# Performance work log

Measured on AMD Instinct MI355X. Metric: run time of the kernel, lower is better.

Reference implementation:

```python
import jax, jax.numpy as jnp
import numpy as np


def _scan_dir(x, A, B, reverse):
    """First-order linear recurrence h_i = A*h_{i-1} + B*x_i along last axis (W).
    x: [Bsz, C, H, W]; A, B: [C]. reverse=True scans right-to-left but returns
    states in original index order (matching torch scan_backward)."""
    xs = jnp.moveaxis(x, -1, 0)  # [W, Bsz, C, H]
    Ab = A[None, :, None]
    Bb = B[None, :, None]
    def step(h, xi):
        h = Ab * h + Bb * xi
        return h, h
    h0 = jnp.zeros_like(xs[0])
    _, hs = jax.lax.scan(step, h0, xs, reverse=reverse)
    return jnp.moveaxis(hs, 0, -1)  # [Bsz, C, H, W]


def _conv1x1(x, W, b):
    # x: [B,Cin,H,W], W: [Cout,Cin], b: [Cout]
    return jnp.einsum('bchw,dc->bdhw', x, W) + b[None, :, None, None]


def setup_inputs() -> dict:
    key = jax.random.key(0)
    ks = jax.random.split(key, 10)
    B, C, H, W = 8, 64, 128, 128
    D = 128  # hidden_dim
    return {
        'F_in': jax.random.normal(ks[0], (B, C, H, W), dtype=jnp.float32),
        'prior': jax.random.uniform(ks[1], (B, 1, H, W), dtype=jnp.float32),
        'Wi': jax.random.normal(ks[2], (D, C), dtype=jnp.float32) * 0.05,
        'bi': jnp.zeros((D,), dtype=jnp.float32),
        'A_param': jax.random.normal(ks[3], (D,), dtype=jnp.float32),
        'B_param': jax.random.normal(ks[4], (D,), dtype=jnp.float32),
        'alpha': jnp.float32(0.1),
        'gamma': jnp.float32(0.1),
        'Wf': jax.random.normal(ks[5], (D, 4 * D), dtype=jnp.float32) * 0.05,
        'bf': jnp.zeros((D,), dtype=jnp.float32),
        'Wo': jax.random.normal(ks[6], (C, D), dtype=jnp.float32) * 0.05,
        'bo': jnp.zeros((C,), dtype=jnp.float32),
    }


def reference(F_in, prior, Wi, bi, A_param, B_param, alpha, gamma, Wf, bf, Wo, bo):
    # prior has 1 channel, repeated to C channels (prior already matches HxW)
    prior_r = jnp.broadcast_to(prior, F_in.shape)
    F_mod = F_in + alpha * prior_r
    x = _conv1x1(F_mod, Wi, bi)  # [B, D, H, W]
    A = jnp.tanh(A_param)
    Bp = B_param
    h_lr = _scan_dir(x, A, Bp, reverse=False)
    h_rl = _scan_dir(x, A, Bp, reverse=True)
    xt = jnp.swapaxes(x, 2, 3)  # scan over H axis
    h_tb = jnp.swapaxes(_scan_dir(xt, A, Bp, reverse=False), 2, 3)
    h_bt = jnp.swapaxes(_scan_dir(xt, A, Bp, reverse=True), 2, 3)
    h = jnp.concatenate([h_lr, h_rl, h_tb, h_bt], axis=1)  # [B, 4D, H, W]
    h = _conv1x1(h, Wf, bf)   # fusion -> [B, D, H, W]
    out = _conv1x1(h, Wo, bo)  # output_proj -> [B, C, H, W]
    return F_mod + gamma * out
```

## Files before the change

kernel.cpp:

```cpp
#include <hip/hip_runtime.h>
#include <hip/hip_bf16.h>

typedef unsigned int u32;
typedef unsigned short u16;
typedef float f32x2 __attribute__((ext_vector_type(2)));
typedef float f32x4 __attribute__((ext_vector_type(4)));
using bf16x8 = __attribute__((ext_vector_type(8))) short;
using f32x4v = __attribute__((ext_vector_type(4))) float;

#define DEVINL __device__ __forceinline__

constexpr int LDS_A = 65536;
constexpr int LDS_B = 32768;
constexpr int XS = 132;
constexpr int LDS_X = 128 * XS * 2;

DEVINL float bf2f(u16 u) { union { u32 i; float f; } v; v.i = ((u32)u) << 16; return v.f; }
DEVINL float bf2f_lo(u32 u) { union { u32 i; float f; } v; v.i = u << 16; return v.f; }
DEVINL float bf2f_hi(u32 u) { union { u32 i; float f; } v; v.i = u & 0xffff0000u; return v.f; }
DEVINL u16 f2bf(float f) {
  __hip_bfloat16 h = __float2bfloat16(f);
  u16 r; __builtin_memcpy(&r, &h, 2); return r;
}
DEVINL u32 pack2(float a, float b) { return (u32)f2bf(a) | ((u32)f2bf(b) << 16); }

__global__ __launch_bounds__(256) void k_pre(
    const float* __restrict__ Wf, const float* __restrict__ Wo,
    const float* __restrict__ bf_, const float* __restrict__ bo,
    const float* __restrict__ A_param, const float* __restrict__ Wi,
    float* __restrict__ A_t, float* __restrict__ beff,
    u16* __restrict__ Mrow, u16* __restrict__ Wi_bf) {
  const int wg = blockIdx.x, t = threadIdx.x;
  if (wg < 128) {
    const int idx = wg * 256 + t;
    const int cout = idx >> 9;
    const int k = idx & 511;
    float s = 0.f;
    for (int d = 0; d < 128; ++d) s = fmaf(Wo[cout * 128 + d], Wf[d * 512 + k], s);
    const int dir = k >> 7, dm = k & 127;
    Mrow[(dir * 64 + cout) * 128 + dm] = f2bf(s);
  } else if (wg == 128) {
    if (t < 128) A_t[t] = tanhf(A_param[t]);
    if (t < 64) {
      float s = bo[t];
      for (int d = 0; d < 128; ++d) s = fmaf(Wo[t * 128 + d], bf_[d], s);
      beff[t] = s;
    }
  } else {
#pragma unroll
    for (int k = 0; k < 32; ++k) {
      const int i = t + k * 256;
      Wi_bf[i] = f2bf(Wi[i]);
    }
  }
}

extern __shared__ char smem[];

template <bool REV, int ROWB>
DEVINL void scan_local(char* buf, int dp, int chunk, f32x2 A2) {
  f32x2 h = { 0.f, 0.f };
  const u32 cb = (u32)(dp * 4);
  const int s = chunk * 32;
  u32 nx[8];
#pragma unroll
  for (int j = 0; j < 8; ++j) {
    const int i = REV ? (127 - (s + j)) : (s + j);
    nx[j] = *(const u32*)(buf + i * ROWB + (cb ^ ((u32)((i & 7) << 4))));
  }
  for (int ib = 0; ib < 32; ib += 8) {
    u32 cur[8];
#pragma unroll
    for (int j = 0; j < 8; ++j) cur[j] = nx[j];
    if (ib + 8 < 32) {
#pragma unroll
      for (int j = 0; j < 8; ++j) {
        const int i2 = s + ib + 8 + j;
        const int i = REV ? (127 - i2) : i2;
        nx[j] = *(const u32*)(buf + i * ROWB + (cb ^ ((u32)((i & 7) << 4))));
      }
    }
#pragma unroll
    for (int j = 0; j < 8; ++j) {
      const int i2 = s + ib + j;
      const int i = REV ? (127 - i2) : i2;
      const f32x2 xv = { bf2f_lo(cur[j]), bf2f_hi(cur[j]) };
      h = A2 * h + xv;
      *(u32*)(buf + i * ROWB + (cb ^ ((u32)((i & 7) << 4)))) = pack2(h.x, h.y);
    }
  }
}

template <bool REV, int ROWB>
DEVINL void scan_fix(char* buf, int dp, int chunk, f32x2 A2) {
  if (chunk == 0) return;
  f32x2 q = A2;
#pragma unroll
  for (int k = 0; k < 5; ++k) q *= q;
  const u32 cb = (u32)(dp * 4);
  f32x2 C = { 0.f, 0.f };
  for (int k = 0; k < chunk; ++k) {
    const int i2 = k * 32 + 31;
    const int i = REV ? (127 - i2) : i2;
    const u32 v = *(const u32*)(buf + i * ROWB + (cb ^ ((u32)((i & 7) << 4))));
    const f32x2 xv = { bf2f_lo(v), bf2f_hi(v) };
    C = C * q + xv;
  }
  f32x2 p = A2;
  const int s = chunk * 32;
  u32 nx[8];
#pragma unroll
  for (int j = 0; j < 8; ++j) {
    const int i = REV ? (127 - (s + j)) : (s + j);
    nx[j] = *(const u32*)(buf + i * ROWB + (cb ^ ((u32)((i & 7) << 4))));
  }
  for (int ib = 0; ib < 32; ib += 8) {
    u32 cur[8];
#pragma unroll
    for (int j = 0; j < 8; ++j) cur[j] = nx[j];
    if (ib + 8 < 32) {
#pragma unroll
      for (int j = 0; j < 8; ++j) {
        const int i2 = s + ib + 8 + j;
        const int i = REV ? (127 - i2) : i2;
        nx[j] = *(const u32*)(buf + i * ROWB + (cb ^ ((u32)((i & 7) << 4))));
      }
    }
#pragma unroll
    for (int j = 0; j < 8; ++j) {
      const int i2 = s + ib + j;
      const int i = REV ? (127 - i2) : i2;
      const f32x2 xv = { bf2f_lo(cur[j]), bf2f_hi(cur[j]) };
      const f32x2 hv = p * C + xv;
      *(u32*)(buf + i * ROWB + (cb ^ ((u32)((i & 7) << 4)))) = pack2(hv.x, hv.y);
      p *= A2;
    }
  }
}

__global__ __launch_bounds__(512, 4) void k_A(
    const float* __restrict__ F_in, const float* __restrict__ prior,
    const u16* __restrict__ Wi_bf, const float* __restrict__ bi,
    const float* __restrict__ Bp, const float* __restrict__ alpha_p,
    const float* __restrict__ A_t, const u16* __restrict__ Mrow,
    u16* __restrict__ x2, u16* __restrict__ Shp) {
  char* bufA = smem;
  char* bufB = smem + 32768;

  const int t = threadIdx.x;
  const int lane = t & 63, wv = t >> 6;
  const int l15 = lane & 15, kg = lane >> 4;
  const int bid = blockIdx.x, b = bid >> 7, h = bid & 127;
  const int wq = wv & 3, eh = wv >> 2;

  {
    const int w = t & 127, ch = t >> 7;
    const float alpha = alpha_p[0];
    const float pv = prior[(b * 128 + h) * 128 + w];
    const float* Fb = F_in + ((size_t)b * 64 + ch * 16) * 16384 + h * 128 + w;
    const u32 sw = (u32)((w & 7) << 4);
    char* rowp = bufA + w * 256;
#pragma unroll
    for (int q = 0; q < 2; ++q) {
      float fv[8];
#pragma unroll
      for (int j = 0; j < 8; ++j) fv[j] = fmaf(alpha, pv, Fb[(q * 8 + j) * 16384]);
      uint4 pk;
      pk.x = pack2(fv[0], fv[1]); pk.y = pack2(fv[2], fv[3]);
      pk.z = pack2(fv[4], fv[5]); pk.w = pack2(fv[6], fv[7]);
      *(uint4*)(rowp + ((u32)(ch * 32 + q * 16) ^ sw)) = pk;
    }
  }
  __syncthreads();

  bf16x8 bF[2][2];
#pragma unroll
  for (int wj = 0; wj < 2; ++wj)
#pragma unroll
    for (int ks = 0; ks < 2; ++ks) {
      const int row = wq * 32 + wj * 16 + l15;
      bF[wj][ks] = *(const bf16x8*)(bufA + row * 256 + ((u32)(ks * 64 + kg * 16) ^ ((u32)((row & 7) << 4))));
    }
  __syncthreads();

  {
    f32x4v acc[4][2];
#pragma unroll
    for (int dt = 0; dt < 4; ++dt) {
      const f32x4 bv = *(const f32x4*)(bi + eh * 64 + dt * 16 + kg * 4);
      const f32x4v bvv = { bv.x, bv.y, bv.z, bv.w };
#pragma unroll
      for (int wj = 0; wj < 2; ++wj) acc[dt][wj] = bvv;
    }
#pragma unroll
    for (int ks = 0; ks < 2; ++ks)
#pragma unroll
      for (int dt = 0; dt < 4; ++dt) {
        const bf16x8 aWi = *(const bf16x8*)(Wi_bf + (eh * 64 + dt * 16 + l15) * 64 + ks * 32 + kg * 8);
        acc[dt][0] = __builtin_amdgcn_mfma_f32_16x16x32_bf16(aWi, bF[0][ks], acc[dt][0], 0, 0, 0);
        acc[dt][1] = __builtin_amdgcn_mfma_f32_16x16x32_bf16(aWi, bF[1][ks], acc[dt][1], 0, 0, 0);
      }
#pragma unroll
    for (int dt = 0; dt < 4; ++dt) {
      const f32x4 B4 = *(const f32x4*)(Bp + eh * 64 + dt * 16 + kg * 4);
      const f32x4v B4v = { B4.x, B4.y, B4.z, B4.w };
#pragma unroll
      for (int wj = 0; wj < 2; ++wj) {
        const f32x4v sv = acc[dt][wj] * B4v;
        const int w = wq * 32 + wj * 16 + l15;
        const int dl = eh * 64 + dt * 16 + kg * 4;
        uint2 pk;
        pk.x = pack2(sv[0], sv[1]);
        pk.y = pack2(sv[2], sv[3]);
        const u32 col = (u32)(dl * 2) ^ ((u32)((w & 7) << 4));
        *(uint2*)(bufA + w * 256 + col) = pk;
        *(uint2*)(bufB + w * 256 + col) = pk;
      }
    }
  }
  __syncthreads();

  {
    u16* xg = x2 + (size_t)bid * 16384;
#pragma unroll
    for (int j = 0; j < 4; ++j) {
      const int idx = t + j * 512;
      const int row = idx >> 4, q = idx & 15;
      const uint4 v = *(const uint4*)(bufA + row * 256 + ((u32)(q * 16) ^ ((u32)((row & 7) << 4))));
      *(uint4*)(xg + row * 128 + q * 8) = v;
    }
  }
  __syncthreads();

  {
    const int sub = t & 255, dp = sub & 63, chunk = sub >> 6, dir = t >> 8;
    const f32x2 a = *(const f32x2*)(A_t + dp * 2);
    char* sb = dir ? bufB : bufA;
    if (dir == 0) scan_local<false, 256>(sb, dp, chunk, a);
    else          scan_local<true , 256>(sb, dp, chunk, a);
    __syncthreads();
    if (dir == 0) scan_fix<false, 256>(sb, dp, chunk, a);
    else          scan_fix<true , 256>(sb, dp, chunk, a);
  }
  __syncthreads();

  f32x4v acc2[2][2];
#pragma unroll
  for (int i = 0; i < 2; ++i)
#pragma unroll
    for (int j = 0; j < 2; ++j) acc2[i][j] = (f32x4v)0.f;
#pragma unroll
  for (int dir = 0; dir < 2; ++dir) {
    const char* buf = dir ? bufB : bufA;
#pragma unroll
    for (int ks = 0; ks < 4; ++ks) {
      bf16x8 afr[2], bfr[2];
#pragma unroll
      for (int ct = 0; ct < 2; ++ct)
        afr[ct] = *(const bf16x8*)(Mrow + ((size_t)dir * 64 + eh * 32 + ct * 16 + l15) * 128 + ks * 32 + kg * 8);
#pragma unroll
      for (int pt = 0; pt < 2; ++pt) {
        const int row = wq * 32 + pt * 16 + l15;
        bfr[pt] = *(const bf16x8*)(buf + row * 256 + ((u32)(ks * 64 + kg * 16) ^ ((u32)((row & 7) << 4))));
      }
#pragma unroll
      for (int ct = 0; ct < 2; ++ct)
#pragma unroll
        for (int pt = 0; pt < 2; ++pt)
          acc2[ct][pt] = __builtin_amdgcn_mfma_f32_16x16x32_bf16(bfr[pt], afr[ct], acc2[ct][pt], 0, 0, 0);
    }
  }
  __syncthreads();

#pragma unroll
  for (int ct = 0; ct < 2; ++ct)
#pragma unroll
    for (int pt = 0; pt < 2; ++pt) {
      const int c = eh * 32 + ct * 16 + l15;
      const int pos = wq * 32 + pt * 16 + kg * 4;
      *(f32x4v*)(smem + c * 512 + ((u32)(pos * 4) ^ ((u32)((c & 7) << 4)))) = acc2[ct][pt];
    }
  __syncthreads();

  {
    u16* og = Shp + (size_t)bid * 8192;
#pragma unroll
    for (int j = 0; j < 8; ++j) {
      const int i = t + j * 512;
      const int c = i >> 6, p2 = (i & 63) * 2;
      const f32x2 v = *(const f32x2*)(smem + c * 512 + ((u32)(p2 * 4) ^ ((u32)((c & 7) << 4))));
      *(u32*)(og + c * 128 + p2) = pack2(v.x, v.y);
    }
  }
}

__global__ __launch_bounds__(256, 5) void k_B(
    const u16* __restrict__ x2,
    const float* __restrict__ A_t, const u16* __restrict__ Mrow,
    u16* __restrict__ Svp) {
  char* bufA = smem;
  char* bufB = smem + 16384;
  const int t = threadIdx.x;
  const int lane = t & 63, wv = t >> 6, l15 = lane & 15, kg = lane >> 4;
  const int bid = blockIdx.x;
  const int b = bid >> 8, w = (bid >> 1) & 127, e = bid & 1;

#pragma unroll
  for (int j = 0; j < 4; ++j) {
    const int idx = t + j * 256;
    const int hh = idx >> 3, q = idx & 7;
    const uint4 v = *(const uint4*)(x2 + ((size_t)(b * 128 + hh) * 128 + w) * 128 + e * 64 + q * 8);
    const u32 col = (u32)(q * 16) ^ ((u32)((hh & 7) << 4));
    *(uint4*)(bufA + hh * 128 + col) = v;
    *(uint4*)(bufB + hh * 128 + col) = v;
  }
  __syncthreads();

  {
    const int dp = t & 31, chunk = (t >> 5) & 3, dir = t >> 7;
    const f32x2 a = *(const f32x2*)(A_t + e * 64 + dp * 2);
    char* sb = dir ? bufB : bufA;
    if (dir == 0) scan_local<false, 128>(sb, dp, chunk, a);
    else          scan_local<true , 128>(sb, dp, chunk, a);
    __syncthreads();
    if (dir == 0) scan_fix<false, 128>(sb, dp, chunk, a);
    else          scan_fix<true , 128>(sb, dp, chunk, a);
  }
  __syncthreads();

  f32x4v acc2[4][2];
#pragma unroll
  for (int i = 0; i < 4; ++i)
#pragma unroll
    for (int j = 0; j < 2; ++j) acc2[i][j] = (f32x4v)0.f;
#pragma unroll
  for (int dir = 0; dir < 2; ++dir) {
    const char* buf = dir ? bufB : bufA;
#pragma unroll
    for (int ks = 0; ks < 2; ++ks) {
      bf16x8 afr[4], bfr[2];
#pragma unroll
      for (int ct = 0; ct < 4; ++ct)
        afr[ct] = *(const bf16x8*)(Mrow + ((size_t)(dir + 2) * 64 + ct * 16 + l15) * 128 + e * 64 + ks * 32 + kg * 8);
#pragma unroll
      for (int pt = 0; pt < 2; ++pt) {
        const int row = wv * 32 + pt * 16 + l15;
        bfr[pt] = *(const bf16x8*)(buf + row * 128 + ((u32)(ks * 64 + kg * 16) ^ ((u32)((row & 7) << 4))));
      }
#pragma unroll
      for (int ct = 0; ct < 4; ++ct)
#pragma unroll
        for (int pt = 0; pt < 2; ++pt)
          acc2[ct][pt] = __builtin_amdgcn_mfma_f32_16x16x32_bf16(bfr[pt], afr[ct], acc2[ct][pt], 0, 0, 0);
    }
  }
  __syncthreads();

#pragma unroll
  for (int ct = 0; ct < 4; ++ct)
#pragma unroll
    for (int pt = 0; pt < 2; ++pt) {
      const int c = ct * 16 + l15;
      const int pos = wv * 32 + pt * 16 + kg * 4;
      *(f32x4v*)(smem + c * 512 + ((u32)(pos * 4) ^ ((u32)((c & 7) << 4)))) = acc2[ct][pt];
    }
  __syncthreads();

  {
    u16* og = Svp + (size_t)bid * 8192;
#pragma unroll
    for (int j = 0; j < 16; ++j) {
      const int i = t + j * 256;
      const int c = i >> 6, p2 = (i & 63) * 2;
      const f32x2 v = *(const f32x2*)(smem + c * 512 + ((u32)(p2 * 4) ^ ((u32)((c & 7) << 4))));
      *(u32*)(og + c * 128 + p2) = pack2(v.x, v.y);
    }
  }
}

__global__ __launch_bounds__(256) void k_final(
    const float* __restrict__ F_in, const float* __restrict__ prior,
    const float* __restrict__ alpha_p, const float* __restrict__ gamma_p,
    const float* __restrict__ beff, const u16* __restrict__ Svp,
    const u16* __restrict__ Shp, float* __restrict__ out) {
  u16* Xu = (u16*)smem;
  const int t = threadIdx.x;
  const int bid = blockIdx.x, b = bid >> 6, c = bid & 63;
  const size_t base = (size_t)bid * 16384;

  for (int i = t; i < 2048; i += 256) {
    const int w = i >> 4, q = i & 15;
    const u16* s0 = Svp + ((size_t)((b * 128 + w) * 2)) * 8192 + c * 128 + q * 8;
    const uint4 a4 = *(const uint4*)(s0);
    const uint4 b4 = *(const uint4*)(s0 + 8192);
    const u16* ap = (const u16*)&a4;
    const u16* bp = (const u16*)&b4;
    u32* dst = (u32*)(Xu + w * 132 + q * 8);
#pragma unroll
    for (int k = 0; k < 4; ++k) {
      const float lo = bf2f(ap[k * 2]) + bf2f(bp[k * 2]);
      const float hi = bf2f(ap[k * 2 + 1]) + bf2f(bp[k * 2 + 1]);
      dst[k] = pack2(lo, hi);
    }
  }
  __syncthreads();
  const float alpha = alpha_p[0], gamma = gamma_p[0];
  const float be = beff[c];
  for (int i = t; i < 2048; i += 256) {
    const int hh = i >> 4, w8 = (i & 15) * 8;
    const size_t off = base + hh * 128 + w8;
    const u16* sh0 = Shp + (size_t)(b * 128 + hh) * 8192 + c * 128 + w8;
    const uint4 g0 = *(const uint4*)(sh0);
    const u16* p0 = (const u16*)&g0;
    const float* Fp = F_in + off;
    float* Op = out + off;
    const float* Pp = prior + (b * 128 + hh) * 128 + w8;
#pragma unroll
    for (int q = 0; q < 8; ++q) {
      const float sv = bf2f(Xu[(w8 + q) * 132 + hh]);
      Op[q] = Fp[q] + alpha * Pp[q] + gamma * (bf2f(p0[q]) + sv + be);
    }
  }
}

extern "C" void kernel_launch(void* const* d_in, const int* in_sizes, int n_in,
                              void* d_out, int out_size, void* d_ws, size_t ws_size,
                              hipStream_t stream) {
  const float* F_in   = (const float*)d_in[0];
  const float* prior  = (const float*)d_in[1];
  const float* Wi     = (const float*)d_in[2];
  const float* bi     = (const float*)d_in[3];
  const float* A_par  = (const float*)d_in[4];
  const float* B_par  = (const float*)d_in[5];
  const float* alpha  = (const float*)d_in[6];
  const float* gamma  = (const float*)d_in[7];
  const float* Wf     = (const float*)d_in[8];
  const float* bf_    = (const float*)d_in[9];
  const float* Wo     = (const float*)d_in[10];
  const float* bo     = (const float*)d_in[11];
  float* out = (float*)d_out;

  char* ws = (char*)d_ws;
  float* A_t   = (float*)ws;
  float* beff  = (float*)(ws + 512);
  u16*   Mrow  = (u16*)(ws + 1024);
  u16*   Wi_bf = (u16*)(ws + 66560);
  u16*   x2    = (u16*)(ws + 82944);
  u16*   Shp   = (u16*)(ws + 82944 + 33554432);
  u16*   Svp   = (u16*)(ws + 82944 + 67108864);

  hipFuncSetAttribute((const void*)k_A, hipFuncAttributeMaxDynamicSharedMemorySize, LDS_A);
  hipFuncSetAttribute((const void*)k_B, hipFuncAttributeMaxDynamicSharedMemorySize, LDS_B);

  k_pre  <<<130, 256, 0, stream>>>(Wf, Wo, bf_, bo, A_par, Wi, A_t, beff, Mrow, Wi_bf);
  k_A    <<<1024, 512, LDS_A, stream>>>(F_in, prior, Wi_bf, bi, B_par, alpha, A_t, Mrow, x2, Shp);
  k_B    <<<2048, 256, LDS_B, stream>>>(x2, A_t, Mrow, Svp);
  k_final<<<512, 256, LDS_X, stream>>>(F_in, prior, alpha, gamma, beff, Svp, Shp, out);
}
```

Measured before the change: 96.86 us.

## Process full hidden dim per block in vertical scan kernel, drop partial-sum merge

The vertical-scan kernel k_B now uses 512-thread blocks that each handle all 128 hidden channels of a column, instead of two 256-thread blocks each handling half the channels and writing separate partial projections. The channel reduction in the projection GEMM is now done entirely inside one block, so Svp holds one bf16 partial instead of two and the final kernel reads half as much Svp data with no add-and-repack. Shared helpers for the scan, GEMM and epilogue are factored out and reused by both kernels. The trade-off is fewer, larger blocks with twice the LDS each, which may lower occupancy.

```diff
diff --git a/kernel.cpp b/kernel.cpp
--- a/kernel.cpp
+++ b/kernel.cpp
@@ -10,8 +10,7 @@
 
 #define DEVINL __device__ __forceinline__
 
-constexpr int LDS_A = 65536;
-constexpr int LDS_B = 32768;
+constexpr int LDS_AB = 65536;
 constexpr int XS = 132;
 constexpr int LDS_X = 128 * XS * 2;
 
@@ -57,7 +56,7 @@
 
 extern __shared__ char smem[];
 
-template <bool REV, int ROWB>
+template <bool REV>
 DEVINL void scan_local(char* buf, int dp, int chunk, f32x2 A2) {
   f32x2 h = { 0.f, 0.f };
   const u32 cb = (u32)(dp * 4);
@@ -66,7 +65,7 @@
 #pragma unroll
   for (int j = 0; j < 8; ++j) {
     const int i = REV ? (127 - (s + j)) : (s + j);
-    nx[j] = *(const u32*)(buf + i * ROWB + (cb ^ ((u32)((i & 7) << 4))));
+    nx[j] = *(const u32*)(buf + i * 256 + (cb ^ ((u32)((i & 7) << 4))));
   }
   for (int ib = 0; ib < 32; ib += 8) {
     u32 cur[8];
@@ -77,7 +76,7 @@
       for (int j = 0; j < 8; ++j) {
         const int i2 = s + ib + 8 + j;
         const int i = REV ? (127 - i2) : i2;
-        nx[j] = *(const u32*)(buf + i * ROWB + (cb ^ ((u32)((i & 7) << 4))));
+        nx[j] = *(const u32*)(buf + i * 256 + (cb ^ ((u32)((i & 7) << 4))));
       }
     }
 #pragma unroll
@@ -86,12 +85,12 @@
       const int i = REV ? (127 - i2) : i2;
       const f32x2 xv = { bf2f_lo(cur[j]), bf2f_hi(cur[j]) };
       h = A2 * h + xv;
-      *(u32*)(buf + i * ROWB + (cb ^ ((u32)((i & 7) << 4)))) = pack2(h.x, h.y);
-    }
-  }
-}
-
-template <bool REV, int ROWB>
+      *(u32*)(buf + i * 256 + (cb ^ ((u32)((i & 7) << 4)))) = pack2(h.x, h.y);
+    }
+  }
+}
+
+template <bool REV>
 DEVINL void scan_fix(char* buf, int dp, int chunk, f32x2 A2) {
   if (chunk == 0) return;
   f32x2 q = A2;
@@ -102,7 +101,7 @@
   for (int k = 0; k < chunk; ++k) {
     const int i2 = k * 32 + 31;
     const int i = REV ? (127 - i2) : i2;
-    const u32 v = *(const u32*)(buf + i * ROWB + (cb ^ ((u32)((i & 7) << 4))));
+    const u32 v = *(const u32*)(buf + i * 256 + (cb ^ ((u32)((i & 7) << 4))));
     const f32x2 xv = { bf2f_lo(v), bf2f_hi(v) };
     C = C * q + xv;
   }
@@ -112,7 +111,7 @@
 #pragma unroll
   for (int j = 0; j < 8; ++j) {
     const int i = REV ? (127 - (s + j)) : (s + j);
-    nx[j] = *(const u32*)(buf + i * ROWB + (cb ^ ((u32)((i & 7) << 4))));
+    nx[j] = *(const u32*)(buf + i * 256 + (cb ^ ((u32)((i & 7) << 4))));
   }
   for (int ib = 0; ib < 32; ib += 8) {
     u32 cur[8];
@@ -123,7 +122,7 @@
       for (int j = 0; j < 8; ++j) {
         const int i2 = s + ib + 8 + j;
         const int i = REV ? (127 - i2) : i2;
-        nx[j] = *(const u32*)(buf + i * ROWB + (cb ^ ((u32)((i & 7) << 4))));
+        nx[j] = *(const u32*)(buf + i * 256 + (cb ^ ((u32)((i & 7) << 4))));
       }
     }
 #pragma unroll
@@ -132,9 +131,66 @@
       const int i = REV ? (127 - i2) : i2;
       const f32x2 xv = { bf2f_lo(cur[j]), bf2f_hi(cur[j]) };
       const f32x2 hv = p * C + xv;
-      *(u32*)(buf + i * ROWB + (cb ^ ((u32)((i & 7) << 4)))) = pack2(hv.x, hv.y);
+      *(u32*)(buf + i * 256 + (cb ^ ((u32)((i & 7) << 4)))) = pack2(hv.x, hv.y);
       p *= A2;
     }
+  }
+}
+
+DEVINL void run_scans512(char* bufA, char* bufB, int t, const float* __restrict__ A_t) {
+  const int sub = t & 255, dp = sub & 63, chunk = sub >> 6, dir = t >> 8;
+  const f32x2 a = *(const f32x2*)(A_t + dp * 2);
+  char* sb = dir ? bufB : bufA;
+  if (dir == 0) scan_local<false>(sb, dp, chunk, a);
+  else          scan_local<true >(sb, dp, chunk, a);
+  __syncthreads();
+  if (dir == 0) scan_fix<false>(sb, dp, chunk, a);
+  else          scan_fix<true >(sb, dp, chunk, a);
+}
+
+DEVINL void combine_full(const char* bufA, const char* bufB, const u16* __restrict__ Mrow,
+                         int dir_base, int eh, int wq, int l15, int kg,
+                         f32x4v (&acc2)[2][2]) {
+#pragma unroll
+  for (int dir = 0; dir < 2; ++dir) {
+    const char* buf = dir ? bufB : bufA;
+#pragma unroll
+    for (int ks = 0; ks < 4; ++ks) {
+      bf16x8 afr[2], bfr[2];
+#pragma unroll
+      for (int ct = 0; ct < 2; ++ct)
+        afr[ct] = *(const bf16x8*)(Mrow + ((size_t)(dir_base + dir) * 64 + eh * 32 + ct * 16 + l15) * 128 + ks * 32 + kg * 8);
+#pragma unroll
+      for (int pt = 0; pt < 2; ++pt) {
+        const int row = wq * 32 + pt * 16 + l15;
+        bfr[pt] = *(const bf16x8*)(buf + row * 256 + ((u32)(ks * 64 + kg * 16) ^ ((u32)((row & 7) << 4))));
+      }
+#pragma unroll
+      for (int ct = 0; ct < 2; ++ct)
+#pragma unroll
+        for (int pt = 0; pt < 2; ++pt)
+          acc2[ct][pt] = __builtin_amdgcn_mfma_f32_16x16x32_bf16(bfr[pt], afr[ct], acc2[ct][pt], 0, 0, 0);
+    }
+  }
+}
+
+DEVINL void outs_epilogue512(const f32x4v (&acc2)[2][2], int eh, int wq, int l15, int kg,
+                             int t, u16* __restrict__ og) {
+#pragma unroll
+  for (int ct = 0; ct < 2; ++ct)
+#pragma unroll
+    for (int pt = 0; pt < 2; ++pt) {
+      const int c = eh * 32 + ct * 16 + l15;
+      const int pos = wq * 32 + pt * 16 + kg * 4;
+      *(f32x4v*)(smem + c * 512 + ((u32)(pos * 4) ^ ((u32)((c & 7) << 4)))) = acc2[ct][pt];
+    }
+  __syncthreads();
+#pragma unroll
+  for (int j = 0; j < 8; ++j) {
+    const int i = t + j * 512;
+    const int c = i >> 6, p2 = (i & 63) * 2;
+    const f32x2 v = *(const f32x2*)(smem + c * 512 + ((u32)(p2 * 4) ^ ((u32)((c & 7) << 4))));
+    *(u32*)(og + c * 128 + p2) = pack2(v.x, v.y);
   }
 }
 
@@ -232,16 +288,7 @@
   }
   __syncthreads();
 
-  {
-    const int sub = t & 255, dp = sub & 63, chunk = sub >> 6, dir = t >> 8;
-    const f32x2 a = *(const f32x2*)(A_t + dp * 2);
-    char* sb = dir ? bufB : bufA;
-    if (dir == 0) scan_local<false, 256>(sb, dp, chunk, a);
-    else          scan_local<true , 256>(sb, dp, chunk, a);
-    __syncthreads();
-    if (dir == 0) scan_fix<false, 256>(sb, dp, chunk, a);
-    else          scan_fix<true , 256>(sb, dp, chunk, a);
-  }
+  run_scans512(bufA, bufB, t, A_t);
   __syncthreads();
 
   f32x4v acc2[2][2];
@@ -249,133 +296,46 @@
   for (int i = 0; i < 2; ++i)
 #pragma unroll
     for (int j = 0; j < 2; ++j) acc2[i][j] = (f32x4v)0.f;
-#pragma unroll
-  for (int dir = 0; dir < 2; ++dir) {
-    const char* buf = dir ? bufB : bufA;
-#pragma unroll
-    for (int ks = 0; ks < 4; ++ks) {
-      bf16x8 afr[2], bfr[2];
-#pragma unroll
-      for (int ct = 0; ct < 2; ++ct)
-        afr[ct] = *(const bf16x8*)(Mrow + ((size_t)dir * 64 + eh * 32 + ct * 16 + l15) * 128 + ks * 32 + kg * 8);
-#pragma unroll
-      for (int pt = 0; pt < 2; ++pt) {
-        const int row = wq * 32 + pt * 16 + l15;
-        bfr[pt] = *(const bf16x8*)(buf + row * 256 + ((u32)(ks * 64 + kg * 16) ^ ((u32)((row & 7) << 4))));
-      }
-#pragma unroll
-      for (int ct = 0; ct < 2; ++ct)
-#pragma unroll
-        for (int pt = 0; pt < 2; ++pt)
-          acc2[ct][pt] = __builtin_amdgcn_mfma_f32_16x16x32_bf16(bfr[pt], afr[ct], acc2[ct][pt], 0, 0, 0);
-    }
-  }
-  __syncthreads();
-
-#pragma unroll
-  for (int ct = 0; ct < 2; ++ct)
-#pragma unroll
-    for (int pt = 0; pt < 2; ++pt) {
-      const int c = eh * 32 + ct * 16 + l15;
-      const int pos = wq * 32 + pt * 16 + kg * 4;
-      *(f32x4v*)(smem + c * 512 + ((u32)(pos * 4) ^ ((u32)((c & 7) << 4)))) = acc2[ct][pt];
-    }
-  __syncthreads();
-
-  {
-    u16* og = Shp + (size_t)bid * 8192;
-#pragma unroll
-    for (int j = 0; j < 8; ++j) {
-      const int i = t + j * 512;
-      const int c = i >> 6, p2 = (i & 63) * 2;
-      const f32x2 v = *(const f32x2*)(smem + c * 512 + ((u32)(p2 * 4) ^ ((u32)((c & 7) << 4))));
-      *(u32*)(og + c * 128 + p2) = pack2(v.x, v.y);
-    }
-  }
-}
-
-__global__ __launch_bounds__(256, 5) void k_B(
+  combine_full(bufA, bufB, Mrow, 0, eh, wq, l15, kg, acc2);
+  __syncthreads();
+  outs_epilogue512(acc2, eh, wq, l15, kg, t, Shp + (size_t)bid * 8192);
+}
+
+__global__ __launch_bounds__(512, 4) void k_B(
     const u16* __restrict__ x2,
     const float* __restrict__ A_t, const u16* __restrict__ Mrow,
     u16* __restrict__ Svp) {
   char* bufA = smem;
-  char* bufB = smem + 16384;
+  char* bufB = smem + 32768;
+
   const int t = threadIdx.x;
-  const int lane = t & 63, wv = t >> 6, l15 = lane & 15, kg = lane >> 4;
-  const int bid = blockIdx.x;
-  const int b = bid >> 8, w = (bid >> 1) & 127, e = bid & 1;
+  const int lane = t & 63, wv = t >> 6;
+  const int l15 = lane & 15, kg = lane >> 4;
+  const int bid = blockIdx.x, b = bid >> 7, w = bid & 127;
+  const int wq = wv & 3, eh = wv >> 2;
 
 #pragma unroll
   for (int j = 0; j < 4; ++j) {
-    const int idx = t + j * 256;
-    const int hh = idx >> 3, q = idx & 7;
-    const uint4 v = *(const uint4*)(x2 + ((size_t)(b * 128 + hh) * 128 + w) * 128 + e * 64 + q * 8);
+    const int idx = t + j * 512;
+    const int hh = idx >> 4, q = idx & 15;
+    const uint4 v = *(const uint4*)(x2 + ((size_t)(b * 128 + hh) * 128 + w) * 128 + q * 8);
     const u32 col = (u32)(q * 16) ^ ((u32)((hh & 7) << 4));
-    *(uint4*)(bufA + hh * 128 + col) = v;
-    *(uint4*)(bufB + hh * 128 + col) = v;
-  }
-  __syncthreads();
-
-  {
-    const int dp = t & 31, chunk = (t >> 5) & 3, dir = t >> 7;
-    const f32x2 a = *(const f32x2*)(A_t + e * 64 + dp * 2);
-    char* sb = dir ? bufB : bufA;
-    if (dir == 0) scan_local<false, 128>(sb, dp, chunk, a);
-    else          scan_local<true , 128>(sb, dp, chunk, a);
-    __syncthreads();
-    if (dir == 0) scan_fix<false, 128>(sb, dp, chunk, a);
-    else          scan_fix<true , 128>(sb, dp, chunk, a);
-  }
-  __syncthreads();
-
-  f32x4v acc2[4][2];
-#pragma unroll
-  for (int i = 0; i < 4; ++i)
+    *(uint4*)(bufA + hh * 256 + col) = v;
+    *(uint4*)(bufB + hh * 256 + col) = v;
+  }
+  __syncthreads();
+
+  run_scans512(bufA, bufB, t, A_t);
+  __syncthreads();
+
+  f32x4v acc2[2][2];
+#pragma unroll
+  for (int i = 0; i < 2; ++i)
 #pragma unroll
     for (int j = 0; j < 2; ++j) acc2[i][j] = (f32x4v)0.f;
-#pragma unroll
-  for (int dir = 0; dir < 2; ++dir) {
-    const char* buf = dir ? bufB : bufA;
-#pragma unroll
-    for (int ks = 0; ks < 2; ++ks) {
-      bf16x8 afr[4], bfr[2];
-#pragma unroll
-      for (int ct = 0; ct < 4; ++ct)
-        afr[ct] = *(const bf16x8*)(Mrow + ((size_t)(dir + 2) * 64 + ct * 16 + l15) * 128 + e * 64 + ks * 32 + kg * 8);
-#pragma unroll
-      for (int pt = 0; pt < 2; ++pt) {
-        const int row = wv * 32 + pt * 16 + l15;
-        bfr[pt] = *(const bf16x8*)(buf + row * 128 + ((u32)(ks * 64 + kg * 16) ^ ((u32)((row & 7) << 4))));
-      }
-#pragma unroll
-      for (int ct = 0; ct < 4; ++ct)
-#pragma unroll
-        for (int pt = 0; pt < 2; ++pt)
-          acc2[ct][pt] = __builtin_amdgcn_mfma_f32_16x16x32_bf16(bfr[pt], afr[ct], acc2[ct][pt], 0, 0, 0);
-    }
-  }
-  __syncthreads();
-
-#pragma unroll
-  for (int ct = 0; ct < 4; ++ct)
-#pragma unroll
-    for (int pt = 0; pt < 2; ++pt) {
-      const int c = ct * 16 + l15;
-      const int pos = wv * 32 + pt * 16 + kg * 4;
-      *(f32x4v*)(smem + c * 512 + ((u32)(pos * 4) ^ ((u32)((c & 7) << 4)))) = acc2[ct][pt];
-    }
-  __syncthreads();
-
-  {
-    u16* og = Svp + (size_t)bid * 8192;
-#pragma unroll
-    for (int j = 0; j < 16; ++j) {
-      const int i = t + j * 256;
-      const int c = i >> 6, p2 = (i & 63) * 2;
-      const f32x2 v = *(const f32x2*)(smem + c * 512 + ((u32)(p2 * 4) ^ ((u32)((c & 7) << 4))));
-      *(u32*)(og + c * 128 + p2) = pack2(v.x, v.y);
-    }
-  }
+  combine_full(bufA, bufB, Mrow, 2, eh, wq, l15, kg, acc2);
+  __syncthreads();
+  outs_epilogue512(acc2, eh, wq, l15, kg, t, Svp + (size_t)bid * 8192);
 }
 
 __global__ __launch_bounds__(256) void k_final(
@@ -390,18 +350,9 @@
 
   for (int i = t; i < 2048; i += 256) {
     const int w = i >> 4, q = i & 15;
-    const u16* s0 = Svp + ((size_t)((b * 128 + w) * 2)) * 8192 + c * 128 + q * 8;
-    const uint4 a4 = *(const uint4*)(s0);
-    const uint4 b4 = *(const uint4*)(s0 + 8192);
-    const u16* ap = (const u16*)&a4;
-    const u16* bp = (const u16*)&b4;
+    const uint4 a4 = *(const uint4*)(Svp + (size_t)(b * 128 + w) * 8192 + c * 128 + q * 8);
     u32* dst = (u32*)(Xu + w * 132 + q * 8);
-#pragma unroll
-    for (int k = 0; k < 4; ++k) {
-      const float lo = bf2f(ap[k * 2]) + bf2f(bp[k * 2]);
-      const float hi = bf2f(ap[k * 2 + 1]) + bf2f(bp[k * 2 + 1]);
-      dst[k] = pack2(lo, hi);
-    }
+    dst[0] = a4.x; dst[1] = a4.y; dst[2] = a4.z; dst[3] = a4.w;
   }
   __syncthreads();
   const float alpha = alpha_p[0], gamma = gamma_p[0];
@@ -409,8 +360,7 @@
   for (int i = t; i < 2048; i += 256) {
     const int hh = i >> 4, w8 = (i & 15) * 8;
     const size_t off = base + hh * 128 + w8;
-    const u16* sh0 = Shp + (size_t)(b * 128 + hh) * 8192 + c * 128 + w8;
-    const uint4 g0 = *(const uint4*)(sh0);
+    const uint4 g0 = *(const uint4*)(Shp + (size_t)(b * 128 + hh) * 8192 + c * 128 + w8);
     const u16* p0 = (const u16*)&g0;
     const float* Fp = F_in + off;
     float* Op = out + off;
@@ -449,11 +399,11 @@
   u16*   Shp   = (u16*)(ws + 82944 + 33554432);
   u16*   Svp   = (u16*)(ws + 82944 + 67108864);
 
-  hipFuncSetAttribute((const void*)k_A, hipFuncAttributeMaxDynamicSharedMemorySize, LDS_A);
-  hipFuncSetAttribute((const void*)k_B, hipFuncAttributeMaxDynamicSharedMemorySize, LDS_B);
+  hipFuncSetAttribute((const void*)k_A, hipFuncAttributeMaxDynamicSharedMemorySize, LDS_AB);
+  hipFuncSetAttribute((const void*)k_B, hipFuncAttributeMaxDynamicSharedMemorySize, LDS_AB);
 
   k_pre  <<<130, 256, 0, stream>>>(Wf, Wo, bf_, bo, A_par, Wi, A_t, beff, Mrow, Wi_bf);
-  k_A    <<<1024, 512, LDS_A, stream>>>(F_in, prior, Wi_bf, bi, B_par, alpha, A_t, Mrow, x2, Shp);
-  k_B    <<<2048, 256, LDS_B, stream>>>(x2, A_t, Mrow, Svp);
+  k_A    <<<1024, 512, LDS_AB, stream>>>(F_in, prior, Wi_bf, bi, B_par, alpha, A_t, Mrow, x2, Shp);
+  k_B    <<<1024, 512, LDS_AB, stream>>>(x2, A_t, Mrow, Svp);
   k_final<<<512, 256, LDS_X, stream>>>(F_in, prior, alpha, gamma, beff, Svp, Shp, out);
 }
```

New measurement: 95.01 us, median of 2. Within noise of the previous version (-1.9%).
